# Kernel tuning notes

Measured on AMD Instinct MI355X. Metric: run time of the kernel, lower is better.

## Reference

```python
import jax, jax.numpy as jnp
import numpy as np


def _pdist2squared(x, y):
    # x: [B, 3, N], y: [B, 3, M] -> squared pairwise dists [B, N, M]
    xx = jnp.sum(x * x, axis=1)[:, :, None]          # [B, N, 1]
    yy = jnp.sum(y * y, axis=1)[:, None, :]          # [B, 1, M]
    dist = xx + yy - 2.0 * jnp.einsum('bdn,bdm->bnm', x, y)
    dist = jnp.where(jnp.isnan(dist), 0.0, dist)     # dist[dist != dist] = 0
    return jnp.maximum(dist, 0.0)                    # clamp to [0, inf)


def setup_inputs() -> dict:
    key = jax.random.key(0)
    k1, k2, k3 = jax.random.split(key, 3)
    B, N, M, C = 4, 16384, 4096, 64
    return {
        'points': jax.random.normal(k1, (B, 3, N), dtype=jnp.float32),
        'new_points': jax.random.normal(k2, (B, 3, M), dtype=jnp.float32),
        'features': jax.random.normal(k3, (B, C, N), dtype=jnp.float32),
        'num_samples': 32,
    }


def reference(points, new_points, features, num_samples):
    # kNN indices: smallest num_samples dists along N for each query m
    dist = _pdist2squared(points, new_points)            # [B, N, M]
    neg = -jnp.transpose(dist, (0, 2, 1))                # [B, M, N]
    _, idx = jax.lax.top_k(neg, num_samples)             # [B, M, K]

    # group_gather_by_index: gather along last axis by idx -> [B, C, M, K]
    def gather(t):
        return jnp.take_along_axis(t[:, :, None, :], idx[:, None, :, :], axis=3)

    grouped_points = gather(points) - new_points[:, :, :, None]   # [B, 3, M, K]
    grouped_features = gather(features)                            # [B, C, M, K]
    return jnp.concatenate([grouped_points, grouped_features], axis=1)
```

## Files before the change

### kernel.cpp

```cpp
#include <hip/hip_runtime.h>

static constexpr int Bn = 4;
static constexpr int Nn = 16384;
static constexpr int Mn = 4096;
static constexpr int Cn = 64;
static constexpr int Kn = 32;

static constexpr int CHUNK   = 2048;
static constexpr int WPB     = 8;
static constexpr int THREADS = WPB * 64;
static constexpr int NCHUNK  = Nn / CHUNK;
static constexpr int NGROUP  = CHUNK / 256;

static constexpr float EPS = 4e-3f;

typedef unsigned long long ull;

__device__ __forceinline__ ull shift_up1(ull v) {
  int lo = __builtin_amdgcn_update_dpp((int)(unsigned)v, (int)(unsigned)v,
                                       0x138, 0xf, 0xf, false);
  int hi = __builtin_amdgcn_update_dpp((int)(v >> 32), (int)(v >> 32),
                                       0x138, 0xf, 0xf, false);
  return ((ull)(unsigned)hi << 32) | (unsigned)lo;
}

__device__ __forceinline__ ull bcast64(ull v, int srclane) {
  unsigned lo = (unsigned)__builtin_amdgcn_readlane((int)(unsigned)v, srclane);
  unsigned hi = (unsigned)__builtin_amdgcn_readlane((int)(v >> 32), srclane);
  return ((ull)hi << 32) | lo;
}

__device__ __forceinline__ void insert_keys(ull kj, ull& lst, ull& tau, int lane) {
  ull mm = __ballot(kj < tau);
  while (mm) {
    const int src = (int)__builtin_ctzll(mm);
    const ull kk = bcast64(kj, src);
    const int pos = (int)__popcll(__ballot(lst < kk));
    const ull sh = shift_up1(lst);
    ull nv = (lane == pos) ? kk : sh;
    nv = (lane < pos) ? lst : nv;
    if (lane < 32) lst = nv;
    tau = bcast64(lst, 31);
    mm &= mm - 1;
    mm &= __ballot(kj < tau);
  }
}

__global__ __launch_bounds__(256) void transpose_f(
    const float* __restrict__ F, float* __restrict__ FT) {
  __shared__ float t[64][65];
  const int tid = threadIdx.x;
  const int bid = blockIdx.x;
  const int xcd = bid & 7;
  const int b   = xcd >> 1;
  const int nt  = (bid >> 3) * 2 + (xcd & 1);
  const float* Fb = F + (size_t)b * Cn * Nn;
  float* FTb = FT + (size_t)b * Nn * Cn;
  for (int sub = 0; sub < 4; ++sub) {
    const int nbase = nt * 256 + sub * 64;
#pragma unroll
    for (int i = 0; i < 16; ++i) {
      const int c = (tid >> 6) + 4 * i;
      t[c][tid & 63] = Fb[(size_t)c * Nn + nbase + (tid & 63)];
    }
    __syncthreads();
#pragma unroll
    for (int i = 0; i < 16; ++i) {
      const int nn = (tid >> 6) + 4 * i;
      FTb[(size_t)(nbase + nn) * Cn + (tid & 63)] = t[tid & 63][nn];
    }
    __syncthreads();
  }
}

__global__ __launch_bounds__(THREADS, 8) void knn_group(
    const float* __restrict__ P,
    const float* __restrict__ Q,
    const float* __restrict__ FT,
    float* __restrict__ out)
{
#pragma clang fp contract(off)
  __shared__ float lds[4][CHUNK];

  const int tid  = threadIdx.x;
  const int lane = tid & 63;
  const int wid  = tid >> 6;
  const int bid  = blockIdx.x;
  const int xcd  = bid & 7;
  const int b    = xcd >> 1;
  const int tile = (bid >> 3) * 2 + (xcd & 1);
  const int m    = tile * WPB + wid;

  const float* Pb = P + (size_t)b * 3 * Nn;
  const float* Qb = Q + (size_t)b * 3 * Mn;

  const float qx = Qb[m];
  const float qy = Qb[Mn + m];
  const float qz = Qb[2 * Mn + m];
  const float yyq = (qx * qx + qy * qy) + qz * qz;

  const int t4 = tid * 4;

  {
    float4 vx = *(const float4*)(Pb + t4);
    float4 vy = *(const float4*)(Pb + Nn + t4);
    float4 vz = *(const float4*)(Pb + 2 * Nn + t4);
    float4 vh;
    vh.x = -0.5f * ((vx.x * vx.x + vy.x * vy.x) + vz.x * vz.x);
    vh.y = -0.5f * ((vx.y * vx.y + vy.y * vy.y) + vz.y * vz.y);
    vh.z = -0.5f * ((vx.z * vx.z + vy.z * vy.z) + vz.z * vz.z);
    vh.w = -0.5f * ((vx.w * vx.w + vy.w * vy.w) + vz.w * vz.w);
    *(float4*)&lds[0][t4] = vx;
    *(float4*)&lds[1][t4] = vy;
    *(float4*)&lds[2][t4] = vz;
    *(float4*)&lds[3][t4] = vh;
  }
  __syncthreads();

  ull lst, tau;
  float tau_f;
  {
    const float x = lds[0][lane];
    const float y = lds[1][lane];
    const float z = lds[2][lane];
    const float h = lds[3][lane];
    const float xx = -2.0f * h;
    const float dot = fmaf(z, qz, fmaf(y, qy, x * qx));
    const float d = fmaxf((xx + yyq) - 2.0f * dot, 0.0f);
    ull key = ((ull)__float_as_uint(d) << 32) | (unsigned)lane;
#pragma unroll
    for (int k = 2; k <= 64; k <<= 1) {
#pragma unroll
      for (int j = k >> 1; j > 0; j >>= 1) {
        const ull other = __shfl_xor(key, j);
        const bool keep_min = ((lane & j) == 0) == ((lane & k) == 0);
        const bool take = keep_min ? (other < key) : (other > key);
        key = take ? other : key;
      }
    }
    lst = (lane < 32) ? key : ~0ull;
    tau = bcast64(lst, 31);
    tau_f = (yyq - __uint_as_float((unsigned)(tau >> 32)) - EPS) * 0.5f;
  }

  for (int ch = 0; ch < NCHUNK; ++ch) {
    const int n0 = ch * CHUNK;

    float4 nx, ny, nz;
    if (ch + 1 < NCHUNK) {
      nx = *(const float4*)(Pb + (n0 + CHUNK) + t4);
      ny = *(const float4*)(Pb + Nn + (n0 + CHUNK) + t4);
      nz = *(const float4*)(Pb + 2 * Nn + (n0 + CHUNK) + t4);
    }

#pragma unroll
    for (int g = 0; g < NGROUP; ++g) {
      const int p = g * 256 + lane * 4;
      const float4 rx = *(const float4*)&lds[0][p];
      const float4 ry = *(const float4*)&lds[1][p];
      const float4 rz = *(const float4*)&lds[2][p];
      const float4 rh = *(const float4*)&lds[3][p];

      float s0 = fmaf(rz.x, qz, fmaf(ry.x, qy, fmaf(rx.x, qx, rh.x)));
      float s1 = fmaf(rz.y, qz, fmaf(ry.y, qy, fmaf(rx.y, qx, rh.y)));
      float s2 = fmaf(rz.z, qz, fmaf(ry.z, qy, fmaf(rx.z, qx, rh.z)));
      float s3 = fmaf(rz.w, qz, fmaf(ry.w, qy, fmaf(rx.w, qx, rh.w)));

      const bool mask_init = (ch == 0) && (g == 0);
      if (mask_init && lane < 16) {
        s0 = s1 = s2 = s3 = -__builtin_inff();
      }

      const float smax = fmaxf(fmaxf(s0, s1), fmaxf(s2, s3));
      if (__any(smax >= tau_f)) {
        const unsigned nb = (unsigned)(n0 + p);
#define PROC(SX, CX, CY, CZ, CH_, NOFF)                                      \
        if (__any(SX >= tau_f)) {                                            \
          const float xx = -2.0f * (CH_);                                    \
          const float dd = fmaf((CZ), qz, fmaf((CY), qy, (CX) * qx));        \
          const float d  = fmaxf((xx + yyq) - 2.0f * dd, 0.0f);              \
          ull key = ((ull)__float_as_uint(d) << 32) | (unsigned)(NOFF);      \
          if (mask_init && lane < 16) key = ~0ull;                           \
          insert_keys(key, lst, tau, lane);                                  \
          tau_f = (yyq - __uint_as_float((unsigned)(tau >> 32)) - EPS) * 0.5f; \
        }
        PROC(s0, rx.x, ry.x, rz.x, rh.x, nb + 0u)
        PROC(s1, rx.y, ry.y, rz.y, rh.y, nb + 1u)
        PROC(s2, rx.z, ry.z, rz.z, rh.z, nb + 2u)
        PROC(s3, rx.w, ry.w, rz.w, rh.w, nb + 3u)
#undef PROC
      }
    }
    __syncthreads();

    if (ch + 1 < NCHUNK) {
      float4 vh;
      vh.x = -0.5f * ((nx.x * nx.x + ny.x * ny.x) + nz.x * nz.x);
      vh.y = -0.5f * ((nx.y * nx.y + ny.y * ny.y) + nz.y * nz.y);
      vh.z = -0.5f * ((nx.z * nx.z + ny.z * ny.z) + nz.z * nz.z);
      vh.w = -0.5f * ((nx.w * nx.w + ny.w * ny.w) + nz.w * nz.w);
      *(float4*)&lds[0][t4] = nx;
      *(float4*)&lds[1][t4] = ny;
      *(float4*)&lds[2][t4] = nz;
      *(float4*)&lds[3][t4] = vh;
      __syncthreads();
    }
  }

  const size_t MK = (size_t)Mn * Kn;
  float* outb = out + (size_t)b * (3 + Cn) * MK;

  if (lane < 32) {
    const int idx = (int)(__shfl(lst, lane) & 0xffffffffull);
    const float px = Pb[idx];
    const float py = Pb[Nn + idx];
    const float pz = Pb[2 * Nn + idx];
    outb[0 * MK + (size_t)m * Kn + lane] = px - qx;
    outb[1 * MK + (size_t)m * Kn + lane] = py - qy;
    outb[2 * MK + (size_t)m * Kn + lane] = pz - qz;
  }

  const float* FTb = FT + (size_t)b * Nn * Cn;
  const int r = lane & 15;
  const int q = lane >> 4;
#pragma unroll
  for (int p2 = 0; p2 < 2; ++p2) {
    const int k = p2 * 16 + r;
    const int idxk = (int)(__shfl(lst, k) & 0xffffffffull);
    const float* row = FTb + (size_t)idxk * Cn;
    float4 v[4];
#pragma unroll
    for (int i = 0; i < 4; ++i)
      v[i] = *(const float4*)(row + (q + 4 * i) * 4);
#pragma unroll
    for (int i = 0; i < 4; ++i) {
      const int c = (q + 4 * i) * 4;
      float* o = outb + (size_t)(3 + c) * MK + (size_t)m * Kn + k;
      o[0 * MK] = v[i].x;
      o[1 * MK] = v[i].y;
      o[2 * MK] = v[i].z;
      o[3 * MK] = v[i].w;
    }
  }
}

extern "C" void kernel_launch(void* const* d_in, const int* in_sizes, int n_in,
                              void* d_out, int out_size, void* d_ws, size_t ws_size,
                              hipStream_t stream) {
  (void)in_sizes; (void)n_in; (void)out_size; (void)ws_size;
  const float* P = (const float*)d_in[0];
  const float* Q = (const float*)d_in[1];
  const float* F = (const float*)d_in[2];
  float* out = (float*)d_out;
  float* FT  = (float*)d_ws;

  hipLaunchKernelGGL(transpose_f, dim3(256), dim3(256), 0, stream, F, FT);
  hipLaunchKernelGGL(knn_group, dim3(Bn * Mn / WPB), dim3(THREADS), 0, stream,
                     P, Q, FT, out);
}
```

Before: 183.3 us.

## Replace per-candidate serial top-k insertion with batched bitonic merge buffer

Replaces the one-key-at-a-time wave insertion into the sorted top-32 list with a pending buffer: candidates that beat the threshold are compacted into a 64-lane buffer via ds_permute and mbcnt, and when it fills the buffer is bitonic-sorted and merged into the top-32 list. It also drops the initial seeding sort, starting from an empty list with an infinite threshold. This is meant to remove the serial ballot/readlane loop cost per candidate, at the expense of a stale threshold between flushes (more candidates admitted) and full 64-wide sorts early on when the threshold is loose.

```diff
diff --git a/kernel.cpp b/kernel.cpp
--- a/kernel.cpp
+++ b/kernel.cpp
@@ -16,34 +16,66 @@
 
 typedef unsigned long long ull;
 
-__device__ __forceinline__ ull shift_up1(ull v) {
-  int lo = __builtin_amdgcn_update_dpp((int)(unsigned)v, (int)(unsigned)v,
-                                       0x138, 0xf, 0xf, false);
-  int hi = __builtin_amdgcn_update_dpp((int)(v >> 32), (int)(v >> 32),
-                                       0x138, 0xf, 0xf, false);
-  return ((ull)(unsigned)hi << 32) | (unsigned)lo;
-}
-
 __device__ __forceinline__ ull bcast64(ull v, int srclane) {
   unsigned lo = (unsigned)__builtin_amdgcn_readlane((int)(unsigned)v, srclane);
   unsigned hi = (unsigned)__builtin_amdgcn_readlane((int)(v >> 32), srclane);
   return ((ull)hi << 32) | lo;
 }
 
-__device__ __forceinline__ void insert_keys(ull kj, ull& lst, ull& tau, int lane) {
-  ull mm = __ballot(kj < tau);
-  while (mm) {
-    const int src = (int)__builtin_ctzll(mm);
-    const ull kk = bcast64(kj, src);
-    const int pos = (int)__popcll(__ballot(lst < kk));
-    const ull sh = shift_up1(lst);
-    ull nv = (lane == pos) ? kk : sh;
-    nv = (lane < pos) ? lst : nv;
-    if (lane < 32) lst = nv;
-    tau = bcast64(lst, 31);
-    mm &= mm - 1;
-    mm &= __ballot(kj < tau);
-  }
+__device__ __forceinline__ int lanes_below(ull m) {
+  return (int)__builtin_amdgcn_mbcnt_hi((unsigned)(m >> 32),
+            __builtin_amdgcn_mbcnt_lo((unsigned)m, 0u));
+}
+
+__device__ __forceinline__ ull permute_push64(int dstlane, ull v) {
+  const int idx = dstlane << 2;
+  int lo = __builtin_amdgcn_ds_permute(idx, (int)(unsigned)v);
+  int hi = __builtin_amdgcn_ds_permute(idx, (int)(v >> 32));
+  return ((ull)(unsigned)hi << 32) | (unsigned)lo;
+}
+
+__device__ __forceinline__ ull sort64_asc(ull key, int lane) {
+#pragma unroll
+  for (int k = 2; k <= 64; k <<= 1) {
+#pragma unroll
+    for (int j = k >> 1; j > 0; j >>= 1) {
+      const ull other = __shfl_xor(key, j);
+      const bool keep_min = ((lane & j) == 0) == ((lane & k) == 0);
+      const bool take = keep_min ? (other < key) : (other > key);
+      key = take ? other : key;
+    }
+  }
+  return key;
+}
+
+__device__ __forceinline__ ull merge_top32(ull lst, ull batch, int lane) {
+  const ull bl = __shfl_xor(batch, 31);
+  ull L = (bl < lst) ? bl : lst;
+#pragma unroll
+  for (int j = 16; j > 0; j >>= 1) {
+    const ull other = __shfl_xor(L, j);
+    const bool keep_min = (lane & j) == 0;
+    const bool take = keep_min ? (other < L) : (other > L);
+    L = take ? other : L;
+  }
+  return (lane < 32) ? L : ~0ull;
+}
+
+__device__ __forceinline__ void set_tauf(ull tau, float yyq, float& tau_f) {
+  const unsigned th = (unsigned)(tau >> 32);
+  tau_f = (th == 0xFFFFFFFFu) ? -__builtin_inff()
+                              : (yyq - __uint_as_float(th) - EPS) * 0.5f;
+}
+
+__device__ __forceinline__ void flush_pend(ull& pend, int& pcnt, ull& lst,
+                                           ull& tau, float& tau_f,
+                                           float yyq, int lane) {
+  const ull key = sort64_asc(pend, lane);
+  lst = merge_top32(lst, key, lane);
+  tau = bcast64(lst, 31);
+  set_tauf(tau, yyq, tau_f);
+  pend = ~0ull;
+  pcnt = 0;
 }
 
 __global__ __launch_bounds__(256) void transpose_f(
@@ -117,31 +149,12 @@
   }
   __syncthreads();
 
-  ull lst, tau;
+  ull lst  = ~0ull;
+  ull tau  = ~0ull;
+  ull pend = ~0ull;
+  int pcnt = 0;
   float tau_f;
-  {
-    const float x = lds[0][lane];
-    const float y = lds[1][lane];
-    const float z = lds[2][lane];
-    const float h = lds[3][lane];
-    const float xx = -2.0f * h;
-    const float dot = fmaf(z, qz, fmaf(y, qy, x * qx));
-    const float d = fmaxf((xx + yyq) - 2.0f * dot, 0.0f);
-    ull key = ((ull)__float_as_uint(d) << 32) | (unsigned)lane;
-#pragma unroll
-    for (int k = 2; k <= 64; k <<= 1) {
-#pragma unroll
-      for (int j = k >> 1; j > 0; j >>= 1) {
-        const ull other = __shfl_xor(key, j);
-        const bool keep_min = ((lane & j) == 0) == ((lane & k) == 0);
-        const bool take = keep_min ? (other < key) : (other > key);
-        key = take ? other : key;
-      }
-    }
-    lst = (lane < 32) ? key : ~0ull;
-    tau = bcast64(lst, 31);
-    tau_f = (yyq - __uint_as_float((unsigned)(tau >> 32)) - EPS) * 0.5f;
-  }
+  set_tauf(tau, yyq, tau_f);
 
   for (int ch = 0; ch < NCHUNK; ++ch) {
     const int n0 = ch * CHUNK;
@@ -161,34 +174,49 @@
       const float4 rz = *(const float4*)&lds[2][p];
       const float4 rh = *(const float4*)&lds[3][p];
 
-      float s0 = fmaf(rz.x, qz, fmaf(ry.x, qy, fmaf(rx.x, qx, rh.x)));
-      float s1 = fmaf(rz.y, qz, fmaf(ry.y, qy, fmaf(rx.y, qx, rh.y)));
-      float s2 = fmaf(rz.z, qz, fmaf(ry.z, qy, fmaf(rx.z, qx, rh.z)));
-      float s3 = fmaf(rz.w, qz, fmaf(ry.w, qy, fmaf(rx.w, qx, rh.w)));
-
-      const bool mask_init = (ch == 0) && (g == 0);
-      if (mask_init && lane < 16) {
-        s0 = s1 = s2 = s3 = -__builtin_inff();
-      }
+      const float s0 = fmaf(rz.x, qz, fmaf(ry.x, qy, fmaf(rx.x, qx, rh.x)));
+      const float s1 = fmaf(rz.y, qz, fmaf(ry.y, qy, fmaf(rx.y, qx, rh.y)));
+      const float s2 = fmaf(rz.z, qz, fmaf(ry.z, qy, fmaf(rx.z, qx, rh.z)));
+      const float s3 = fmaf(rz.w, qz, fmaf(ry.w, qy, fmaf(rx.w, qx, rh.w)));
 
       const float smax = fmaxf(fmaxf(s0, s1), fmaxf(s2, s3));
       if (__any(smax >= tau_f)) {
         const unsigned nb = (unsigned)(n0 + p);
-#define PROC(SX, CX, CY, CZ, CH_, NOFF)                                      \
-        if (__any(SX >= tau_f)) {                                            \
-          const float xx = -2.0f * (CH_);                                    \
-          const float dd = fmaf((CZ), qz, fmaf((CY), qy, (CX) * qx));        \
-          const float d  = fmaxf((xx + yyq) - 2.0f * dd, 0.0f);              \
-          ull key = ((ull)__float_as_uint(d) << 32) | (unsigned)(NOFF);      \
-          if (mask_init && lane < 16) key = ~0ull;                           \
-          insert_keys(key, lst, tau, lane);                                  \
-          tau_f = (yyq - __uint_as_float((unsigned)(tau >> 32)) - EPS) * 0.5f; \
+#define SUBW(SX, CX, CY, CZ, CH_, NOFF)                                       \
+        {                                                                     \
+          ull mj = __ballot((SX) >= tau_f);                                   \
+          if (mj) {                                                           \
+            const float xxv = -2.0f * (CH_);                                  \
+            const float ddv = fmaf((CZ), qz, fmaf((CY), qy, (CX) * qx));      \
+            const float dv  = fmaxf((xxv + yyq) - 2.0f * ddv, 0.0f);          \
+            const ull kj = ((ull)__float_as_uint(dv) << 32) | (unsigned)(NOFF);\
+            int c = (int)__popcll(mj);                                        \
+            if (pcnt + c > 63) {                                              \
+              flush_pend(pend, pcnt, lst, tau, tau_f, yyq, lane);             \
+              mj = __ballot((SX) >= tau_f);                                   \
+              c  = (int)__popcll(mj);                                         \
+            }                                                                 \
+            if (c > 63) {                  \
+              const ull key = sort64_asc(kj, lane);                           \
+              lst = merge_top32(lst, key, lane);                              \
+              tau = bcast64(lst, 31);                                         \
+              set_tauf(tau, yyq, tau_f);                                      \
+            } else if (c) {                                                   \
+              const int prefix = lanes_below(mj);                             \
+              const bool pass = (mj >> lane) & 1ull;                          \
+              const int dst = pass ? (pcnt + prefix) : 63;                    \
+              const ull got = permute_push64(dst, kj);                        \
+              const bool take = (lane >= pcnt) && (lane < pcnt + c);          \
+              pend = take ? got : pend;                                       \
+              pcnt += c;                                                      \
+            }                                                                 \
+          }                                                                   \
         }
-        PROC(s0, rx.x, ry.x, rz.x, rh.x, nb + 0u)
-        PROC(s1, rx.y, ry.y, rz.y, rh.y, nb + 1u)
-        PROC(s2, rx.z, ry.z, rz.z, rh.z, nb + 2u)
-        PROC(s3, rx.w, ry.w, rz.w, rh.w, nb + 3u)
-#undef PROC
+        SUBW(s0, rx.x, ry.x, rz.x, rh.x, nb + 0u)
+        SUBW(s1, rx.y, ry.y, rz.y, rh.y, nb + 1u)
+        SUBW(s2, rx.z, ry.z, rz.z, rh.z, nb + 2u)
+        SUBW(s3, rx.w, ry.w, rz.w, rh.w, nb + 3u)
+#undef SUBW
       }
     }
     __syncthreads();
@@ -207,6 +235,8 @@
     }
   }
 
+  if (pcnt > 0) flush_pend(pend, pcnt, lst, tau, tau_f, yyq, lane);
+
   const size_t MK = (size_t)Mn * Kn;
   float* outb = out + (size_t)b * (3 + Cn) * MK;
 
```

After: 226.7 us. +23.7%, slower.

## Process two queries per wave with split u32 keys and direct global-to-LDS loads

Applied to the files above, without the earlier changes.

Each wavefront now handles two query points, so each LDS read of candidate coordinates is reused for both queries and half as many blocks are launched. The 64-bit packed key list becomes separate 32-bit distance and index registers, and insertion walks candidates per lane group rather than using a ballot loop on 64-bit keys. The bitonic-sort seeding is replaced by an infinite initial threshold. Point coordinates are copied with global_load_lds into a three-row LDS buffer, and the squared norm is recomputed from it rather than stored. This removes the register-staged prefetch that overlapped the next chunk's load with compute, and it raises register pressure per wave.

```diff
diff --git a/kernel.cpp b/kernel.cpp
--- a/kernel.cpp
+++ b/kernel.cpp
@@ -8,6 +8,7 @@
 
 static constexpr int CHUNK   = 2048;
 static constexpr int WPB     = 8;
+static constexpr int QPW     = 2;
 static constexpr int THREADS = WPB * 64;
 static constexpr int NCHUNK  = Nn / CHUNK;
 static constexpr int NGROUP  = CHUNK / 256;
@@ -15,35 +16,54 @@
 static constexpr float EPS = 4e-3f;
 
 typedef unsigned long long ull;
-
-__device__ __forceinline__ ull shift_up1(ull v) {
-  int lo = __builtin_amdgcn_update_dpp((int)(unsigned)v, (int)(unsigned)v,
-                                       0x138, 0xf, 0xf, false);
-  int hi = __builtin_amdgcn_update_dpp((int)(v >> 32), (int)(v >> 32),
-                                       0x138, 0xf, 0xf, false);
-  return ((ull)(unsigned)hi << 32) | (unsigned)lo;
-}
-
-__device__ __forceinline__ ull bcast64(ull v, int srclane) {
-  unsigned lo = (unsigned)__builtin_amdgcn_readlane((int)(unsigned)v, srclane);
-  unsigned hi = (unsigned)__builtin_amdgcn_readlane((int)(v >> 32), srclane);
-  return ((ull)hi << 32) | lo;
-}
-
-__device__ __forceinline__ void insert_keys(ull kj, ull& lst, ull& tau, int lane) {
-  ull mm = __ballot(kj < tau);
-  while (mm) {
-    const int src = (int)__builtin_ctzll(mm);
-    const ull kk = bcast64(kj, src);
-    const int pos = (int)__popcll(__ballot(lst < kk));
-    const ull sh = shift_up1(lst);
-    ull nv = (lane == pos) ? kk : sh;
-    nv = (lane < pos) ? lst : nv;
-    if (lane < 32) lst = nv;
-    tau = bcast64(lst, 31);
-    mm &= mm - 1;
-    mm &= __ballot(kj < tau);
-  }
+typedef unsigned int u32;
+
+__device__ __forceinline__ u32 dpp_shr1(u32 v) {
+  return (u32)__builtin_amdgcn_update_dpp((int)v, (int)v, 0x138, 0xf, 0xf, false);
+}
+__device__ __forceinline__ u32 rdlane(u32 v, int l) {
+  return (u32)__builtin_amdgcn_readlane((int)v, l);
+}
+
+__device__ __forceinline__ void gl_lds16(const float* g, float* l) {
+  __builtin_amdgcn_global_load_lds(
+      (const __attribute__((address_space(1))) void*)g,
+      (__attribute__((address_space(3))) void*)l, 16, 0, 0);
+}
+
+__device__ __forceinline__ void insert_one(u32 kd, u32 ki,
+                                           u32& lst_d, u32& lst_i,
+                                           u32& tau_d, int lane) {
+  const int pos = (int)__popcll(__ballot(lst_d <= kd));
+  const u32 shd = dpp_shr1(lst_d);
+  const u32 shi = dpp_shr1(lst_i);
+  u32 nd = (lane == pos) ? kd : shd;
+  u32 ni = (lane == pos) ? ki : shi;
+  nd = (lane < pos) ? lst_d : nd;
+  ni = (lane < pos) ? lst_i : ni;
+  if (lane < 32) { lst_d = nd; lst_i = ni; }
+  tau_d = rdlane(lst_d, 31);
+}
+
+__device__ __forceinline__ void insert_grp(ull mAny, u32 d0, u32 d1, u32 d2,
+                                           u32 d3, u32 sb,
+                                           u32& lst_d, u32& lst_i,
+                                           u32& tau_d, int lane) {
+  while (mAny) {
+    const int src = (int)__builtin_ctzll(mAny);
+    mAny &= mAny - 1;
+    const u32 ib = sb + ((u32)src << 2);
+    u32 kd;
+    kd = rdlane(d0, src); if (kd < tau_d) insert_one(kd, ib + 0u, lst_d, lst_i, tau_d, lane);
+    kd = rdlane(d1, src); if (kd < tau_d) insert_one(kd, ib + 1u, lst_d, lst_i, tau_d, lane);
+    kd = rdlane(d2, src); if (kd < tau_d) insert_one(kd, ib + 2u, lst_d, lst_i, tau_d, lane);
+    kd = rdlane(d3, src); if (kd < tau_d) insert_one(kd, ib + 3u, lst_d, lst_i, tau_d, lane);
+  }
+}
+
+__device__ __forceinline__ float tf_of(u32 tau_d, float yyq) {
+  return (tau_d == 0xFFFFFFFFu) ? -__builtin_inff()
+                                : (yyq - __uint_as_float(tau_d) - EPS) * 0.5f;
 }
 
 __global__ __launch_bounds__(256) void transpose_f(
@@ -80,7 +100,7 @@
     float* __restrict__ out)
 {
 #pragma clang fp contract(off)
-  __shared__ float lds[4][CHUNK];
+  __shared__ float lds[3][CHUNK];
 
   const int tid  = threadIdx.x;
   const int lane = tid & 63;
@@ -89,69 +109,35 @@
   const int xcd  = bid & 7;
   const int b    = xcd >> 1;
   const int tile = (bid >> 3) * 2 + (xcd & 1);
-  const int m    = tile * WPB + wid;
+  const int m0   = tile * (WPB * QPW) + wid * QPW;
 
   const float* Pb = P + (size_t)b * 3 * Nn;
   const float* Qb = Q + (size_t)b * 3 * Mn;
 
-  const float qx = Qb[m];
-  const float qy = Qb[Mn + m];
-  const float qz = Qb[2 * Mn + m];
-  const float yyq = (qx * qx + qy * qy) + qz * qz;
-
-  const int t4 = tid * 4;
-
-  {
-    float4 vx = *(const float4*)(Pb + t4);
-    float4 vy = *(const float4*)(Pb + Nn + t4);
-    float4 vz = *(const float4*)(Pb + 2 * Nn + t4);
-    float4 vh;
-    vh.x = -0.5f * ((vx.x * vx.x + vy.x * vy.x) + vz.x * vz.x);
-    vh.y = -0.5f * ((vx.y * vx.y + vy.y * vy.y) + vz.y * vz.y);
-    vh.z = -0.5f * ((vx.z * vx.z + vy.z * vy.z) + vz.z * vz.z);
-    vh.w = -0.5f * ((vx.w * vx.w + vy.w * vy.w) + vz.w * vz.w);
-    *(float4*)&lds[0][t4] = vx;
-    *(float4*)&lds[1][t4] = vy;
-    *(float4*)&lds[2][t4] = vz;
-    *(float4*)&lds[3][t4] = vh;
-  }
-  __syncthreads();
-
-  ull lst, tau;
-  float tau_f;
-  {
-    const float x = lds[0][lane];
-    const float y = lds[1][lane];
-    const float z = lds[2][lane];
-    const float h = lds[3][lane];
-    const float xx = -2.0f * h;
-    const float dot = fmaf(z, qz, fmaf(y, qy, x * qx));
-    const float d = fmaxf((xx + yyq) - 2.0f * dot, 0.0f);
-    ull key = ((ull)__float_as_uint(d) << 32) | (unsigned)lane;
-#pragma unroll
-    for (int k = 2; k <= 64; k <<= 1) {
-#pragma unroll
-      for (int j = k >> 1; j > 0; j >>= 1) {
-        const ull other = __shfl_xor(key, j);
-        const bool keep_min = ((lane & j) == 0) == ((lane & k) == 0);
-        const bool take = keep_min ? (other < key) : (other > key);
-        key = take ? other : key;
-      }
-    }
-    lst = (lane < 32) ? key : ~0ull;
-    tau = bcast64(lst, 31);
-    tau_f = (yyq - __uint_as_float((unsigned)(tau >> 32)) - EPS) * 0.5f;
-  }
+  const float2 qxv = *(const float2*)(Qb + m0);
+  const float2 qyv = *(const float2*)(Qb + Mn + m0);
+  const float2 qzv = *(const float2*)(Qb + 2 * Mn + m0);
+  const float qx0 = qxv.x, qx1 = qxv.y;
+  const float qy0 = qyv.x, qy1 = qyv.y;
+  const float qz0 = qzv.x, qz1 = qzv.y;
+  const float yyq0 = (qx0 * qx0 + qy0 * qy0) + qz0 * qz0;
+  const float yyq1 = (qx1 * qx1 + qy1 * qy1) + qz1 * qz1;
+
+  u32 lst_d0 = 0xFFFFFFFFu, lst_i0 = 0u, tau_d0 = 0xFFFFFFFFu;
+  u32 lst_d1 = 0xFFFFFFFFu, lst_i1 = 0u, tau_d1 = 0xFFFFFFFFu;
+  float tf0 = -__builtin_inff(), tf1 = -__builtin_inff();
 
   for (int ch = 0; ch < NCHUNK; ++ch) {
     const int n0 = ch * CHUNK;
 
-    float4 nx, ny, nz;
-    if (ch + 1 < NCHUNK) {
-      nx = *(const float4*)(Pb + (n0 + CHUNK) + t4);
-      ny = *(const float4*)(Pb + Nn + (n0 + CHUNK) + t4);
-      nz = *(const float4*)(Pb + 2 * Nn + (n0 + CHUNK) + t4);
-    }
+    {
+      const int base = wid * 256;
+      const float* g0 = Pb + n0 + base + lane * 4;
+      gl_lds16(g0,          &lds[0][base]);
+      gl_lds16(g0 + Nn,     &lds[1][base]);
+      gl_lds16(g0 + 2 * Nn, &lds[2][base]);
+    }
+    __syncthreads();
 
 #pragma unroll
     for (int g = 0; g < NGROUP; ++g) {
@@ -159,87 +145,109 @@
       const float4 rx = *(const float4*)&lds[0][p];
       const float4 ry = *(const float4*)&lds[1][p];
       const float4 rz = *(const float4*)&lds[2][p];
-      const float4 rh = *(const float4*)&lds[3][p];
-
-      float s0 = fmaf(rz.x, qz, fmaf(ry.x, qy, fmaf(rx.x, qx, rh.x)));
-      float s1 = fmaf(rz.y, qz, fmaf(ry.y, qy, fmaf(rx.y, qx, rh.y)));
-      float s2 = fmaf(rz.z, qz, fmaf(ry.z, qy, fmaf(rx.z, qx, rh.z)));
-      float s3 = fmaf(rz.w, qz, fmaf(ry.w, qy, fmaf(rx.w, qx, rh.w)));
-
-      const bool mask_init = (ch == 0) && (g == 0);
-      if (mask_init && lane < 16) {
-        s0 = s1 = s2 = s3 = -__builtin_inff();
+
+      float4 h;
+      h.x = -0.5f * ((rx.x * rx.x + ry.x * ry.x) + rz.x * rz.x);
+      h.y = -0.5f * ((rx.y * rx.y + ry.y * ry.y) + rz.y * rz.y);
+      h.z = -0.5f * ((rx.z * rx.z + ry.z * ry.z) + rz.z * rz.z);
+      h.w = -0.5f * ((rx.w * rx.w + ry.w * ry.w) + rz.w * rz.w);
+
+      const float a0 = fmaf(rz.x, qz0, fmaf(ry.x, qy0, fmaf(rx.x, qx0, h.x)));
+      const float a1 = fmaf(rz.y, qz0, fmaf(ry.y, qy0, fmaf(rx.y, qx0, h.y)));
+      const float a2 = fmaf(rz.z, qz0, fmaf(ry.z, qy0, fmaf(rx.z, qx0, h.z)));
+      const float a3 = fmaf(rz.w, qz0, fmaf(ry.w, qy0, fmaf(rx.w, qx0, h.w)));
+      const float b0 = fmaf(rz.x, qz1, fmaf(ry.x, qy1, fmaf(rx.x, qx1, h.x)));
+      const float b1 = fmaf(rz.y, qz1, fmaf(ry.y, qy1, fmaf(rx.y, qx1, h.y)));
+      const float b2 = fmaf(rz.z, qz1, fmaf(ry.z, qy1, fmaf(rx.z, qx1, h.z)));
+      const float b3 = fmaf(rz.w, qz1, fmaf(ry.w, qy1, fmaf(rx.w, qx1, h.w)));
+
+      const float ga = fmaxf(fmaxf(a0, a1), fmaxf(a2, a3));
+      const float gb = fmaxf(fmaxf(b0, b1), fmaxf(b2, b3));
+      const ull mA = __ballot(ga >= tf0);
+      const ull mB = __ballot(gb >= tf1);
+
+      if (mA | mB) {
+        const float xx0 = -2.0f * h.x;
+        const float xx1 = -2.0f * h.y;
+        const float xx2 = -2.0f * h.z;
+        const float xx3 = -2.0f * h.w;
+        const u32 sb = (u32)(n0 + g * 256);
+
+        if (mA) {
+          float dd, dv;
+          u32 e0, e1, e2, e3;
+          dd = fmaf(rz.x, qz0, fmaf(ry.x, qy0, rx.x * qx0));
+          dv = fmaxf((xx0 + yyq0) - 2.0f * dd, 0.0f); e0 = __float_as_uint(dv);
+          dd = fmaf(rz.y, qz0, fmaf(ry.y, qy0, rx.y * qx0));
+          dv = fmaxf((xx1 + yyq0) - 2.0f * dd, 0.0f); e1 = __float_as_uint(dv);
+          dd = fmaf(rz.z, qz0, fmaf(ry.z, qy0, rx.z * qx0));
+          dv = fmaxf((xx2 + yyq0) - 2.0f * dd, 0.0f); e2 = __float_as_uint(dv);
+          dd = fmaf(rz.w, qz0, fmaf(ry.w, qy0, rx.w * qx0));
+          dv = fmaxf((xx3 + yyq0) - 2.0f * dd, 0.0f); e3 = __float_as_uint(dv);
+          insert_grp(mA, e0, e1, e2, e3, sb, lst_d0, lst_i0, tau_d0, lane);
+          tf0 = tf_of(tau_d0, yyq0);
+        }
+        if (mB) {
+          float dd, dv;
+          u32 e0, e1, e2, e3;
+          dd = fmaf(rz.x, qz1, fmaf(ry.x, qy1, rx.x * qx1));
+          dv = fmaxf((xx0 + yyq1) - 2.0f * dd, 0.0f); e0 = __float_as_uint(dv);
+          dd = fmaf(rz.y, qz1, fmaf(ry.y, qy1, rx.y * qx1));
+          dv = fmaxf((xx1 + yyq1) - 2.0f * dd, 0.0f); e1 = __float_as_uint(dv);
+          dd = fmaf(rz.z, qz1, fmaf(ry.z, qy1, rx.z * qx1));
+          dv = fmaxf((xx2 + yyq1) - 2.0f * dd, 0.0f); e2 = __float_as_uint(dv);
+          dd = fmaf(rz.w, qz1, fmaf(ry.w, qy1, rx.w * qx1));
+          dv = fmaxf((xx3 + yyq1) - 2.0f * dd, 0.0f); e3 = __float_as_uint(dv);
+          insert_grp(mB, e0, e1, e2, e3, sb, lst_d1, lst_i1, tau_d1, lane);
+          tf1 = tf_of(tau_d1, yyq1);
+        }
       }
-
-      const float smax = fmaxf(fmaxf(s0, s1), fmaxf(s2, s3));
-      if (__any(smax >= tau_f)) {
-        const unsigned nb = (unsigned)(n0 + p);
-#define PROC(SX, CX, CY, CZ, CH_, NOFF)                                      \
-        if (__any(SX >= tau_f)) {                                            \
-          const float xx = -2.0f * (CH_);                                    \
-          const float dd = fmaf((CZ), qz, fmaf((CY), qy, (CX) * qx));        \
-          const float d  = fmaxf((xx + yyq) - 2.0f * dd, 0.0f);              \
-          ull key = ((ull)__float_as_uint(d) << 32) | (unsigned)(NOFF);      \
-          if (mask_init && lane < 16) key = ~0ull;                           \
-          insert_keys(key, lst, tau, lane);                                  \
-          tau_f = (yyq - __uint_as_float((unsigned)(tau >> 32)) - EPS) * 0.5f; \
-        }
-        PROC(s0, rx.x, ry.x, rz.x, rh.x, nb + 0u)
-        PROC(s1, rx.y, ry.y, rz.y, rh.y, nb + 1u)
-        PROC(s2, rx.z, ry.z, rz.z, rh.z, nb + 2u)
-        PROC(s3, rx.w, ry.w, rz.w, rh.w, nb + 3u)
-#undef PROC
-      }
-    }
-    __syncthreads();
-
-    if (ch + 1 < NCHUNK) {
-      float4 vh;
-      vh.x = -0.5f * ((nx.x * nx.x + ny.x * ny.x) + nz.x * nz.x);
-      vh.y = -0.5f * ((nx.y * nx.y + ny.y * ny.y) + nz.y * nz.y);
-      vh.z = -0.5f * ((nx.z * nx.z + ny.z * ny.z) + nz.z * nz.z);
-      vh.w = -0.5f * ((nx.w * nx.w + ny.w * ny.w) + nz.w * nz.w);
-      *(float4*)&lds[0][t4] = nx;
-      *(float4*)&lds[1][t4] = ny;
-      *(float4*)&lds[2][t4] = nz;
-      *(float4*)&lds[3][t4] = vh;
-      __syncthreads();
-    }
+    }
+    __syncthreads();
   }
 
   const size_t MK = (size_t)Mn * Kn;
   float* outb = out + (size_t)b * (3 + Cn) * MK;
-
-  if (lane < 32) {
-    const int idx = (int)(__shfl(lst, lane) & 0xffffffffull);
-    const float px = Pb[idx];
-    const float py = Pb[Nn + idx];
-    const float pz = Pb[2 * Nn + idx];
-    outb[0 * MK + (size_t)m * Kn + lane] = px - qx;
-    outb[1 * MK + (size_t)m * Kn + lane] = py - qy;
-    outb[2 * MK + (size_t)m * Kn + lane] = pz - qz;
-  }
-
   const float* FTb = FT + (size_t)b * Nn * Cn;
-  const int r = lane & 15;
-  const int q = lane >> 4;
-#pragma unroll
-  for (int p2 = 0; p2 < 2; ++p2) {
-    const int k = p2 * 16 + r;
-    const int idxk = (int)(__shfl(lst, k) & 0xffffffffull);
-    const float* row = FTb + (size_t)idxk * Cn;
-    float4 v[4];
-#pragma unroll
-    for (int i = 0; i < 4; ++i)
-      v[i] = *(const float4*)(row + (q + 4 * i) * 4);
-#pragma unroll
-    for (int i = 0; i < 4; ++i) {
-      const int c = (q + 4 * i) * 4;
-      float* o = outb + (size_t)(3 + c) * MK + (size_t)m * Kn + k;
-      o[0 * MK] = v[i].x;
-      o[1 * MK] = v[i].y;
-      o[2 * MK] = v[i].z;
-      o[3 * MK] = v[i].w;
+
+#pragma unroll
+  for (int q = 0; q < QPW; ++q) {
+    const int m = m0 + q;
+    const u32 lsti = q ? lst_i1 : lst_i0;
+    const float qx = q ? qx1 : qx0;
+    const float qy = q ? qy1 : qy0;
+    const float qz = q ? qz1 : qz0;
+
+    if (lane < 32) {
+      const int idx = (int)__shfl((int)lsti, lane);
+      const float px = Pb[idx];
+      const float py = Pb[Nn + idx];
+      const float pz = Pb[2 * Nn + idx];
+      outb[0 * MK + (size_t)m * Kn + lane] = px - qx;
+      outb[1 * MK + (size_t)m * Kn + lane] = py - qy;
+      outb[2 * MK + (size_t)m * Kn + lane] = pz - qz;
+    }
+
+    const int r  = lane & 15;
+    const int qh = lane >> 4;
+#pragma unroll
+    for (int p2 = 0; p2 < 2; ++p2) {
+      const int k = p2 * 16 + r;
+      const int idxk = (int)__shfl((int)lsti, k);
+      const float* row = FTb + (size_t)idxk * Cn;
+      float4 v[4];
+#pragma unroll
+      for (int i = 0; i < 4; ++i)
+        v[i] = *(const float4*)(row + (qh + 4 * i) * 4);
+#pragma unroll
+      for (int i = 0; i < 4; ++i) {
+        const int c = (qh + 4 * i) * 4;
+        float* o = outb + (size_t)(3 + c) * MK + (size_t)m * Kn + k;
+        o[0 * MK] = v[i].x;
+        o[1 * MK] = v[i].y;
+        o[2 * MK] = v[i].z;
+        o[3 * MK] = v[i].w;
+      }
     }
   }
 }
@@ -255,6 +263,6 @@
   float* FT  = (float*)d_ws;
 
   hipLaunchKernelGGL(transpose_f, dim3(256), dim3(256), 0, stream, F, FT);
-  hipLaunchKernelGGL(knn_group, dim3(Bn * Mn / WPB), dim3(THREADS), 0, stream,
-                     P, Q, FT, out);
-}
+  hipLaunchKernelGGL(knn_group, dim3(Bn * Mn / (WPB * QPW)), dim3(THREADS), 0,
+                     stream, P, Q, FT, out);
+}
```

Result: slower. 274.5 us (+49.8%).

## Track 40 candidates by 32-bit score, re-sort exact distances at end

Applied to the files above, without the earlier changes.

The running kNN list now holds 40 slots keyed on the cheap dot-product score (split into float score and u32 index registers) instead of 32 slots of 64-bit exact-distance keys. The epsilon-padded threshold is dropped. Insertion works on 32-bit values with a single DPP shift, and candidate lanes are walked with readlane. At the end, the exact distances of the 40 survivors are recomputed and bitonic-sorted to pick the top 32. This cuts per-insert cost but relies on 8 spare slots to absorb rounding differences between the score ordering and the reference distance ordering, and lowers the occupancy hint from 8 to 6.

```diff
diff --git a/kernel.cpp b/kernel.cpp
--- a/kernel.cpp
+++ b/kernel.cpp
@@ -11,39 +11,47 @@
 static constexpr int THREADS = WPB * 64;
 static constexpr int NCHUNK  = Nn / CHUNK;
 static constexpr int NGROUP  = CHUNK / 256;
-
-static constexpr float EPS = 4e-3f;
+static constexpr int LSLOTS  = 40;
 
 typedef unsigned long long ull;
-
-__device__ __forceinline__ ull shift_up1(ull v) {
-  int lo = __builtin_amdgcn_update_dpp((int)(unsigned)v, (int)(unsigned)v,
-                                       0x138, 0xf, 0xf, false);
-  int hi = __builtin_amdgcn_update_dpp((int)(v >> 32), (int)(v >> 32),
-                                       0x138, 0xf, 0xf, false);
-  return ((ull)(unsigned)hi << 32) | (unsigned)lo;
-}
-
-__device__ __forceinline__ ull bcast64(ull v, int srclane) {
-  unsigned lo = (unsigned)__builtin_amdgcn_readlane((int)(unsigned)v, srclane);
-  unsigned hi = (unsigned)__builtin_amdgcn_readlane((int)(v >> 32), srclane);
-  return ((ull)hi << 32) | lo;
-}
-
-__device__ __forceinline__ void insert_keys(ull kj, ull& lst, ull& tau, int lane) {
-  ull mm = __ballot(kj < tau);
-  while (mm) {
-    const int src = (int)__builtin_ctzll(mm);
-    const ull kk = bcast64(kj, src);
-    const int pos = (int)__popcll(__ballot(lst < kk));
-    const ull sh = shift_up1(lst);
-    ull nv = (lane == pos) ? kk : sh;
-    nv = (lane < pos) ? lst : nv;
-    if (lane < 32) lst = nv;
-    tau = bcast64(lst, 31);
-    mm &= mm - 1;
-    mm &= __ballot(kj < tau);
-  }
+typedef unsigned int u32;
+
+__device__ __forceinline__ u32 dpp_shr1(u32 v) {
+  return (u32)__builtin_amdgcn_update_dpp((int)v, (int)v, 0x138, 0xf, 0xf, false);
+}
+__device__ __forceinline__ u32 rdlane(u32 v, int l) {
+  return (u32)__builtin_amdgcn_readlane((int)v, l);
+}
+__device__ __forceinline__ float rdlane_f(float v, int l) {
+  return __uint_as_float(rdlane(__float_as_uint(v), l));
+}
+
+__device__ __forceinline__ ull sort64_asc(ull key, int lane) {
+#pragma unroll
+  for (int k = 2; k <= 64; k <<= 1) {
+#pragma unroll
+    for (int j = k >> 1; j > 0; j >>= 1) {
+      const ull other = __shfl_xor(key, j);
+      const bool keep_min = ((lane & j) == 0) == ((lane & k) == 0);
+      const bool take = keep_min ? (other < key) : (other > key);
+      key = take ? other : key;
+    }
+  }
+  return key;
+}
+
+__device__ __forceinline__ void insert40(float kj, u32 ki,
+                                         float& lst_s, u32& lst_i,
+                                         float& tau_s, int lane) {
+  const int pos = (int)__popcll(__ballot(lst_s >= kj));
+  const float shd = __uint_as_float(dpp_shr1(__float_as_uint(lst_s)));
+  const u32  shi = dpp_shr1(lst_i);
+  float nd = (lane == pos) ? kj : shd;
+  u32   ni = (lane == pos) ? ki : shi;
+  nd = (lane < pos) ? lst_s : nd;
+  ni = (lane < pos) ? lst_i : ni;
+  if (lane < LSLOTS) { lst_s = nd; lst_i = ni; }
+  tau_s = rdlane_f(lst_s, LSLOTS - 1);
 }
 
 __global__ __launch_bounds__(256) void transpose_f(
@@ -73,7 +81,7 @@
   }
 }
 
-__global__ __launch_bounds__(THREADS, 8) void knn_group(
+__global__ __launch_bounds__(THREADS, 6) void knn_group(
     const float* __restrict__ P,
     const float* __restrict__ Q,
     const float* __restrict__ FT,
@@ -100,6 +108,10 @@
   const float yyq = (qx * qx + qy * qy) + qz * qz;
 
   const int t4 = tid * 4;
+
+  float lst_s = -__builtin_inff();
+  u32   lst_i = 0u;
+  float tau_s = -__builtin_inff();
 
   {
     float4 vx = *(const float4*)(Pb + t4);
@@ -117,30 +129,20 @@
   }
   __syncthreads();
 
-  ull lst, tau;
-  float tau_f;
   {
     const float x = lds[0][lane];
     const float y = lds[1][lane];
     const float z = lds[2][lane];
     const float h = lds[3][lane];
-    const float xx = -2.0f * h;
-    const float dot = fmaf(z, qz, fmaf(y, qy, x * qx));
-    const float d = fmaxf((xx + yyq) - 2.0f * dot, 0.0f);
-    ull key = ((ull)__float_as_uint(d) << 32) | (unsigned)lane;
-#pragma unroll
-    for (int k = 2; k <= 64; k <<= 1) {
-#pragma unroll
-      for (int j = k >> 1; j > 0; j >>= 1) {
-        const ull other = __shfl_xor(key, j);
-        const bool keep_min = ((lane & j) == 0) == ((lane & k) == 0);
-        const bool take = keep_min ? (other < key) : (other > key);
-        key = take ? other : key;
-      }
-    }
-    lst = (lane < 32) ? key : ~0ull;
-    tau = bcast64(lst, 31);
-    tau_f = (yyq - __uint_as_float((unsigned)(tau >> 32)) - EPS) * 0.5f;
+    const float s = fmaf(z, qz, fmaf(y, qy, fmaf(x, qx, h)));
+    const u32 sb = __float_as_uint(s);
+    const u32 os = sb ^ (((int)sb < 0) ? 0xFFFFFFFFu : 0x80000000u);
+    ull key = (((ull)(~os)) << 32) | (u32)lane;
+    key = sort64_asc(key, lane);
+    const int i0 = (int)(key & 0xFFFFFFFFull);
+    const float sv = __shfl(s, i0);
+    if (lane < LSLOTS) { lst_s = sv; lst_i = (u32)i0; }
+    tau_s = rdlane_f(lst_s, LSLOTS - 1);
   }
 
   for (int ch = 0; ch < NCHUNK; ++ch) {
@@ -166,29 +168,28 @@
       float s2 = fmaf(rz.z, qz, fmaf(ry.z, qy, fmaf(rx.z, qx, rh.z)));
       float s3 = fmaf(rz.w, qz, fmaf(ry.w, qy, fmaf(rx.w, qx, rh.w)));
 
-      const bool mask_init = (ch == 0) && (g == 0);
-      if (mask_init && lane < 16) {
+      if (ch == 0 && g == 0 && lane < 16) {
         s0 = s1 = s2 = s3 = -__builtin_inff();
       }
 
       const float smax = fmaxf(fmaxf(s0, s1), fmaxf(s2, s3));
-      if (__any(smax >= tau_f)) {
-        const unsigned nb = (unsigned)(n0 + p);
-#define PROC(SX, CX, CY, CZ, CH_, NOFF)                                      \
-        if (__any(SX >= tau_f)) {                                            \
-          const float xx = -2.0f * (CH_);                                    \
-          const float dd = fmaf((CZ), qz, fmaf((CY), qy, (CX) * qx));        \
-          const float d  = fmaxf((xx + yyq) - 2.0f * dd, 0.0f);              \
-          ull key = ((ull)__float_as_uint(d) << 32) | (unsigned)(NOFF);      \
-          if (mask_init && lane < 16) key = ~0ull;                           \
-          insert_keys(key, lst, tau, lane);                                  \
-          tau_f = (yyq - __uint_as_float((unsigned)(tau >> 32)) - EPS) * 0.5f; \
-        }
-        PROC(s0, rx.x, ry.x, rz.x, rh.x, nb + 0u)
-        PROC(s1, rx.y, ry.y, rz.y, rh.y, nb + 1u)
-        PROC(s2, rx.z, ry.z, rz.z, rh.z, nb + 2u)
-        PROC(s3, rx.w, ry.w, rz.w, rh.w, nb + 3u)
-#undef PROC
+      ull mm = __ballot(smax > tau_s);
+      if (mm) {
+        const u32 nb = (u32)(n0 + g * 256);
+        do {
+          const int src = (int)__builtin_ctzll(mm);
+          mm &= mm - 1;
+          const u32 ib = nb + ((u32)src << 2);
+          float k;
+          k = rdlane_f(s0, src);
+          if (k > tau_s) insert40(k, ib + 0u, lst_s, lst_i, tau_s, lane);
+          k = rdlane_f(s1, src);
+          if (k > tau_s) insert40(k, ib + 1u, lst_s, lst_i, tau_s, lane);
+          k = rdlane_f(s2, src);
+          if (k > tau_s) insert40(k, ib + 2u, lst_s, lst_i, tau_s, lane);
+          k = rdlane_f(s3, src);
+          if (k > tau_s) insert40(k, ib + 3u, lst_s, lst_i, tau_s, lane);
+        } while (mm);
       }
     }
     __syncthreads();
@@ -207,11 +208,26 @@
     }
   }
 
+  ull key;
+  {
+    const int idx = (int)lst_i;
+    const float x = Pb[idx];
+    const float y = Pb[Nn + idx];
+    const float z = Pb[2 * Nn + idx];
+    const float xx = (x * x + y * y) + z * z;
+    const float dot = fmaf(z, qz, fmaf(y, qy, x * qx));
+    const float d = fmaxf((xx + yyq) - 2.0f * dot, 0.0f);
+    key = (lane < LSLOTS)
+            ? ((((ull)__float_as_uint(d)) << 32) | (u32)idx)
+            : ~0ull;
+    key = sort64_asc(key, lane);
+  }
+
   const size_t MK = (size_t)Mn * Kn;
   float* outb = out + (size_t)b * (3 + Cn) * MK;
 
   if (lane < 32) {
-    const int idx = (int)(__shfl(lst, lane) & 0xffffffffull);
+    const int idx = (int)(key & 0xFFFFFFFFull);
     const float px = Pb[idx];
     const float py = Pb[Nn + idx];
     const float pz = Pb[2 * Nn + idx];
@@ -221,20 +237,20 @@
   }
 
   const float* FTb = FT + (size_t)b * Nn * Cn;
-  const int r = lane & 15;
-  const int q = lane >> 4;
+  const int r  = lane & 15;
+  const int qh = lane >> 4;
 #pragma unroll
   for (int p2 = 0; p2 < 2; ++p2) {
     const int k = p2 * 16 + r;
-    const int idxk = (int)(__shfl(lst, k) & 0xffffffffull);
+    const int idxk = (int)(__shfl(key, k) & 0xFFFFFFFFull);
     const float* row = FTb + (size_t)idxk * Cn;
     float4 v[4];
 #pragma unroll
     for (int i = 0; i < 4; ++i)
-      v[i] = *(const float4*)(row + (q + 4 * i) * 4);
+      v[i] = *(const float4*)(row + (qh + 4 * i) * 4);
 #pragma unroll
     for (int i = 0; i < 4; ++i) {
-      const int c = (q + 4 * i) * 4;
+      const int c = (qh + 4 * i) * 4;
       float* o = outb + (size_t)(3 + c) * MK + (size_t)m * Kn + k;
       o[0 * MK] = v[i].x;
       o[1 * MK] = v[i].y;
```

Result: slower. 249.9 us (+36.4%).
